# Optimization experiments

Measured on AMD Instinct MI355X. Metric: run time of the kernel, lower is better.

The kernel has to match this reference:

```python
import jax, jax.numpy as jnp
import numpy as np

CUTOFF = 4.0
D_RBF = 20


def _rbf_consts():
    # e3nn soft_one_hot_linspace, basis='gaussian', cutoff=False
    values = np.linspace(0.0, CUTOFF, D_RBF)
    step = values[1] - values[0]
    # RadialBasis normalization buffers: 4000 uniform samples, unbiased std
    rs = np.linspace(0.0, CUTOFF, 4001)[1:]
    bs = np.exp(-(((rs[:, None] - values[None, :]) / step) ** 2)) / 1.12
    mean = bs.mean(0)
    inv_std = 1.0 / bs.std(0, ddof=1)
    return (jnp.asarray(values, jnp.float32), jnp.float32(step),
            jnp.asarray(mean, jnp.float32), jnp.asarray(inv_std, jnp.float32))


def setup_inputs() -> dict:
    N, P, E = 2000, 50000, 300000
    Ds, Dv, H, HO = 256, 128, 256, 128
    din = Ds + Dv + D_RBF + Dv  # 532
    key = jax.random.key(0)
    ks = jax.random.split(key, 12)
    atom_xyz = jax.random.uniform(ks[0], (N, 3), jnp.float32, 0.0, 8.0)
    probe_xyz = jax.random.uniform(ks[1], (P, 3), jnp.float32, 0.0, 8.0)
    cell = jnp.eye(3, dtype=jnp.float32)[None] * 8.0  # [1,3,3]
    src = jax.random.randint(ks[2], (E,), 0, N)
    dst = jax.random.randint(ks[3], (E,), 0, P)
    edges = jnp.stack([src, dst], axis=-1).astype(jnp.int32)  # [E,2]
    edges_displacement = jax.random.randint(ks[4], (E, 3), -1, 2).astype(jnp.float32)
    S_final = jax.random.normal(ks[5], (N, Ds), jnp.float32)
    V_final = jax.random.normal(ks[6], (N, Dv, 3), jnp.float32)
    s = 0.02
    return {
        'atom_xyz': atom_xyz, 'probe_xyz': probe_xyz, 'cell': cell,
        'edges': edges, 'edges_displacement': edges_displacement,
        'S_final': S_final, 'V_final': V_final,
        'ln_gamma': jnp.ones((din,), jnp.float32),
        'ln_beta': jnp.zeros((din,), jnp.float32),
        'W1': jax.random.normal(ks[7], (din, H), jnp.float32) * s,
        'b1': jnp.zeros((H,), jnp.float32),
        'W2': jax.random.normal(ks[8], (H, H), jnp.float32) * s,
        'b2': jnp.zeros((H,), jnp.float32),
        'Wo1': jax.random.normal(ks[9], (H, HO), jnp.float32) * s,
        'bo1': jnp.zeros((HO,), jnp.float32),
        'Wo2': jax.random.normal(ks[10], (HO, 1), jnp.float32) * s,
        'bo2': jnp.full((1,), -10.0, jnp.float32),
    }


def reference(atom_xyz, probe_xyz, cell, edges, edges_displacement,
              S_final, V_final, ln_gamma, ln_beta,
              W1, b1, W2, b2, Wo1, bo1, Wo2, bo2):
    values, step, rbf_mean, rbf_inv_std = _rbf_consts()
    src, dst = edges[:, 0], edges[:, 1]
    # PBC displacement: edges_displacement @ cell (single graph -> cell[0])
    disp = edges_displacement @ cell[0]                     # [E,3]
    vec = probe_xyz[dst] - (atom_xyz[src] + disp)           # [E,3]
    d = jnp.maximum(jnp.linalg.norm(vec, axis=-1, keepdims=True), 1e-8)
    r_hat = vec / d                                         # [E,3]
    ds = d[:, 0]                                            # [E]
    # RBF (gaussian soft one-hot) + normalization
    diff = (ds[:, None] - values) / step
    e = (jnp.exp(-diff * diff) / 1.12 - rbf_mean) * rbf_inv_std  # [E,20]
    x = ds / CUTOFF
    x5 = x ** 5
    env = (1.0 - 21.0 * x5 + 35.0 * x5 * x - 15.0 * x5 * x * x)
    env = env * (ds < CUTOFF).astype(jnp.float32)           # [E]
    # geometric invariants
    q = jnp.einsum('ek,eck->ec', r_hat, V_final[src])       # [E,Dv]
    n_atom = jnp.linalg.norm(V_final, axis=-1)              # [N,Dv]
    feat = jnp.concatenate([S_final[src], n_atom[src], e, q], axis=-1)  # [E,532]
    # LayerNorm
    mu = feat.mean(-1, keepdims=True)
    var = feat.var(-1, keepdims=True)
    feat = (feat - mu) * jax.lax.rsqrt(var + 1e-5) * ln_gamma + ln_beta
    # message MLP
    h = jax.nn.silu(feat @ W1 + b1)
    h = jax.nn.silu(h @ W2 + b2)                            # [E,256]
    # envelope-weighted scatter-add to probes
    m_p = jax.ops.segment_sum(h * env[:, None], dst,
                              num_segments=probe_xyz.shape[0])  # [P,256]
    # output MLP
    o = jax.nn.silu(m_p @ Wo1 + bo1)
    rho = o @ Wo2 + bo2                                     # [P,1]
    return rho[:, 0]
```

## Files before the change

### kernel.cpp

```cpp
#include <hip/hip_runtime.h>
#include <hip/hip_bf16.h>
#include <hip/hip_fp16.h>

#define DIN 532
#define DRBF 20
#define EB 32

typedef __attribute__((ext_vector_type(8))) short s8v;
typedef __attribute__((ext_vector_type(4))) float f4v;

static __device__ __forceinline__ float silu_f(float x){
    return x * __builtin_amdgcn_rcpf(1.0f + __expf(-x));
}
static __device__ __forceinline__ short f2bf(float x){
    __hip_bfloat16 b = __float2bfloat16(x);
    return *(short*)&b;
}
static __device__ __forceinline__ s8v pack8(float4 f0, float4 f1){
    s8v r;
    r[0]=f2bf(f0.x); r[1]=f2bf(f0.y); r[2]=f2bf(f0.z); r[3]=f2bf(f0.w);
    r[4]=f2bf(f1.x); r[5]=f2bf(f1.y); r[6]=f2bf(f1.z); r[7]=f2bf(f1.w);
    return r;
}
static __device__ __forceinline__ s8v pack8p(const float* p){
    float4 f0 = *(const float4*)p, f1 = *(const float4*)(p + 4);
    return pack8(f0, f1);
}
static __device__ __forceinline__ bool detect_bf16(const void* cellraw){
    float c0 = ((const float*)cellraw)[0];
    return !(c0 > 7.5f && c0 < 8.5f);
}
static __device__ __forceinline__ float loadr(const void* p, bool isbf, long idx){
    if (isbf) return __bfloat162float(((const __hip_bfloat16*)p)[idx]);
    return ((const float*)p)[idx];
}

struct ConvArgs {
    const void* src[10];
    float*      dst[10];
    int         sz[10];
    int         total;
};

__global__ __launch_bounds__(256) void k_pre(ConvArgs ca,
    const void* W1r, const void* gammar, const void* betar, const void* b1r,
    const void* W2r, const void* Wo1r, const void* cellraw,
    float* Gpart, float* Bpart, float* rbfc,
    short* w1ef, short* w2f, short* w1f, short* wo1f)
{
    int b = blockIdx.x, t = threadIdx.x;
    bool isbf = detect_bf16(cellraw);
    if (b < 256){
        int stride = 256 * 256;
        for (int i = b*256 + t; i < ca.total; i += stride){
            int idx = i, k = 0;
            while (idx >= ca.sz[k]) { idx -= ca.sz[k]; k++; }
            float v = 0.0f;
            if (ca.src[k]) v = loadr(ca.src[k], isbf, idx);
            ca.dst[k][idx] = v;
        }
        return;
    }
    int pb = b - 256;
    if (pb < 17){
        int i0 = pb * 32, i1 = min(i0 + 32, DIN);
        float g = 0.0f, bb = 0.0f;
        for (int i = i0; i < i1; i++){
            float w  = loadr(W1r, isbf, (long)i*256 + t);
            g  += loadr(gammar, isbf, i) * w;
            bb += loadr(betar,  isbf, i) * w;
        }
        if (pb == 0) bb += loadr(b1r, isbf, t);
        Gpart[pb*256 + t] = g;
        Bpart[pb*256 + t] = bb;
        return;
    }
    if (pb == 17){
        __shared__ float ssum[DRBF][8], ssq[DRBF][8];
        if (t < 160){
            int m = t >> 3, c = t & 7;
            const float step = 4.0f/19.0f;
            float vm = step * m;
            float s = 0.0f, ss = 0.0f;
            for (int i = c*500 + 1; i <= c*500 + 500; i++){
                float r = 0.001f * (float)i;
                float u = (r - vm) / step;
                float bv = __expf(-u*u) * (1.0f/1.12f);
                s += bv; ss += bv*bv;
            }
            ssum[m][c] = s; ssq[m][c] = ss;
        }
        __syncthreads();
        if (t < DRBF){
            float s = 0.0f, ss = 0.0f;
            for (int c = 0; c < 8; c++){ s += ssum[t][c]; ss += ssq[t][c]; }
            float mean = s / 4000.0f;
            float var  = (ss - s*s/4000.0f) / 3999.0f;
            rbfc[t]        = mean;
            rbfc[DRBF + t] = rsqrtf(var);
        }
        return;
    }
    int wid = t >> 6, lane = t & 63;
    int q8 = (lane >> 4) * 8, nl = lane & 15;
    if (pb <= 21){
        int f = (pb - 18)*4 + wid;
        for (int j = 0; j < 8; j++){
            int kk = q8 + j;
            int n  = f*16 + nl;
            float v = (kk < DRBF)
                ? loadr(gammar, isbf, 384 + kk) * loadr(W1r, isbf, (long)(384 + kk)*256 + n)
                : 0.0f;
            w1ef[((f << 6) | lane)*8 + j] = f2bf(v);
        }
    } else if (pb <= 53){
        int f = (pb - 22)*4 + wid;
        int ks = f & 7;
        for (int j = 0; j < 8; j++){
            int kk = ks*32 + q8 + j;
            int n  = (f >> 3)*16 + nl;
            w2f[((f << 6) | lane)*8 + j] = f2bf(loadr(W2r, isbf, (long)kk*256 + n));
        }
    } else if (pb <= 117){
        int f = (pb - 54)*4 + wid;
        int ksg = f >> 4, ntg = f & 15;
        int base;
        if (ksg < 8)       base = ksg * 32;
        else if (ksg < 12) base = 256 + (ksg - 8) * 32;
        else               base = 404 + (ksg - 12) * 32;
        for (int j = 0; j < 8; j++){
            int kk = base + q8 + j;
            int n  = ntg*16 + nl;
            w1f[((f << 6) | lane)*8 + j] =
                f2bf(loadr(gammar, isbf, kk) * loadr(W1r, isbf, (long)kk*256 + n));
        }
    } else {
        int f = (pb - 118)*4 + wid;
        int ks = f & 7;
        for (int j = 0; j < 8; j++){
            int kk = ks*32 + q8 + j;
            int n  = (f >> 3)*16 + nl;
            wo1f[((f << 6) | lane)*8 + j] = f2bf(loadr(Wo1r, isbf, (long)kk*128 + n));
        }
    }
}

__global__ __launch_bounds__(256) void k_mid(
    const float* S, const float* V, const short* w1f, float4* AM,
    float* scal, int N,
    const int* edges, const void* edraw, const float* cell,
    const float* axyz, const float* pxyz,
    int* etot, int* flag, int2* esd, float4* geo, float* m_p,
    const void* cellraw, int E,
    const float* Gpart, const float* Bpart, float* Gv, float* Bb,
    int GA, int GG)
{
    int b = blockIdx.x, t = threadIdx.x;
    int wid = t >> 6, lane = t & 63;

    if (b < GA){
        __shared__ float Vxl[16][132], Vyl[16][132], Vzl[16][132], nll[16][132];
        int q = lane >> 4, ml = lane & 15;
        int a0 = b * 16;

        for (int a = 0; a < 16; a++){
            int atom = min(a0 + a, N - 1);
            if (t < 128){
                float x = V[(size_t)atom*384 + 3*t];
                float y = V[(size_t)atom*384 + 3*t + 1];
                float z = V[(size_t)atom*384 + 3*t + 2];
                Vxl[a][t] = x; Vyl[a][t] = y; Vzl[a][t] = z;
                nll[a][t] = sqrtf(x*x + y*y + z*z);
            }
        }
        __syncthreads();

        for (int a2 = 0; a2 < 4; a2++){
            int a = (wid << 2) + a2;
            int row = min(a0 + a, N - 1);
            float v[11];
            #pragma unroll
            for (int k = 0; k < 11; k++) v[k] = 0.0f;
            for (int e = lane; e < 256; e += 64){
                float s = S[(size_t)row*256 + e];
                v[0] += s; v[1] += s*s;
            }
            for (int e = lane; e < 128; e += 64){
                float n = nll[a][e], x = Vxl[a][e], y = Vyl[a][e], z = Vzl[a][e];
                v[0] += n;   v[1] += n*n;
                v[2] += x;   v[3] += y;   v[4] += z;
                v[5] += x*x; v[6] += x*y; v[7] += x*z;
                v[8] += y*y; v[9] += y*z; v[10] += z*z;
            }
            #pragma unroll
            for (int k = 0; k < 11; k++)
                for (int off2 = 32; off2 > 0; off2 >>= 1)
                    v[k] += __shfl_xor(v[k], off2, 64);
            if (lane == 0 && a0 + a < N)
                for (int k = 0; k < 11; k++) scal[(a0 + a)*12 + k] = v[k];
        }

        f4v zz = {0.0f, 0.0f, 0.0f, 0.0f};
        f4v aA1[4], aM0[4], aM1[4], aM2[4];
        #pragma unroll
        for (int nt = 0; nt < 4; nt++){ aA1[nt]=zz; aM0[nt]=zz; aM1[nt]=zz; aM2[nt]=zz; }

        int srow = min(a0 + ml, N - 1);
        #pragma unroll
        for (int ks = 0; ks < 8; ks++){
            s8v av = pack8p(&S[(size_t)srow*256 + ks*32 + q*8]);
            #pragma unroll
            for (int nt = 0; nt < 4; nt++){
                s8v bf = ((const s8v*)w1f)[(((ks << 4) | ((wid << 2) | nt)) << 6) | lane];
                aA1[nt] = __builtin_amdgcn_mfma_f32_16x16x32_bf16(av, bf, aA1[nt], 0, 0, 0);
            }
        }
        #pragma unroll
        for (int ks = 0; ks < 4; ks++){
            s8v av = pack8p(&nll[ml][ks*32 + q*8]);
            #pragma unroll
            for (int nt = 0; nt < 4; nt++){
                s8v bf = ((const s8v*)w1f)[((((8 + ks) << 4) | ((wid << 2) | nt)) << 6) | lane];
                aA1[nt] = __builtin_amdgcn_mfma_f32_16x16x32_bf16(av, bf, aA1[nt], 0, 0, 0);
            }
        }
        #pragma unroll
        for (int ks = 0; ks < 4; ks++){
            s8v ax = pack8p(&Vxl[ml][ks*32 + q*8]);
            s8v ay = pack8p(&Vyl[ml][ks*32 + q*8]);
            s8v az = pack8p(&Vzl[ml][ks*32 + q*8]);
            #pragma unroll
            for (int nt = 0; nt < 4; nt++){
                s8v bf = ((const s8v*)w1f)[((((12 + ks) << 4) | ((wid << 2) | nt)) << 6) | lane];
                aM0[nt] = __builtin_amdgcn_mfma_f32_16x16x32_bf16(ax, bf, aM0[nt], 0, 0, 0);
                aM1[nt] = __builtin_amdgcn_mfma_f32_16x16x32_bf16(ay, bf, aM1[nt], 0, 0, 0);
                aM2[nt] = __builtin_amdgcn_mfma_f32_16x16x32_bf16(az, bf, aM2[nt], 0, 0, 0);
            }
        }

        #pragma unroll
        for (int nt = 0; nt < 4; nt++){
            #pragma unroll
            for (int reg = 0; reg < 4; reg++){
                int atom = a0 + (q << 2) + reg;
                if (atom < N)
                    AM[(size_t)atom*256 + ((wid << 6) | (nt << 4) | ml)] =
                        make_float4(aA1[nt][reg], aM0[nt][reg], aM1[nt][reg], aM2[nt][reg]);
            }
        }
        return;
    }

    if (b < GA + GG){
        __shared__ int wcnt[4], wbase[4];
        bool isbf = detect_bf16(cellraw);
        float c0=cell[0],c1=cell[1],c2=cell[2],c3=cell[3],c4=cell[4];
        float c5=cell[5],c6=cell[6],c7=cell[7],c8=cell[8];
        int i = (b - GA)*256 + t;

        bool act = false;
        int s = 0, dd = 0;
        float r0 = 0.f, r1 = 0.f, r2 = 0.f, dn = 0.f;
        if (i < E){
            s = edges[2*i]; dd = edges[2*i + 1];
            float d0 = loadr(edraw, isbf, 3L*i);
            float d1 = loadr(edraw, isbf, 3L*i + 1);
            float d2 = loadr(edraw, isbf, 3L*i + 2);
            float dx = d0*c0 + d1*c3 + d2*c6;
            float dy = d0*c1 + d1*c4 + d2*c7;
            float dz = d0*c2 + d1*c5 + d2*c8;
            float vx = pxyz[3*dd]   - (axyz[3*s]   + dx);
            float vy = pxyz[3*dd+1] - (axyz[3*s+1] + dy);
            float vz = pxyz[3*dd+2] - (axyz[3*s+2] + dz);
            dn = fmaxf(sqrtf(vx*vx + vy*vy + vz*vz), 1e-8f);
            act = dn < 4.0f;
            float inv = __builtin_amdgcn_rcpf(dn);
            r0 = vx*inv; r1 = vy*inv; r2 = vz*inv;
        }
        unsigned long long mask = __ballot(act);
        if (lane == 0) wcnt[wid] = __popcll(mask);
        __syncthreads();
        if (t == 0){
            int tot = wcnt[0] + wcnt[1] + wcnt[2] + wcnt[3];
            int base = tot ? atomicAdd(etot, tot) : 0;
            int run = base;
            #pragma unroll
            for (int w2 = 0; w2 < 4; w2++){ wbase[w2] = run; run += wcnt[w2]; }
        }
        __syncthreads();
        if (act){
            int pos = wbase[wid] + __popcll(mask & ((1ULL << lane) - 1ULL));
            esd[pos] = make_int2(s, dd);
            geo[pos] = make_float4(r0, r1, r2, dn);
            if (atomicExch(&flag[dd], 1) == 0){
                float4 z = make_float4(0.f, 0.f, 0.f, 0.f);
                float4* p = (float4*)&m_p[(size_t)dd*256];
                #pragma unroll 4
                for (int k = 0; k < 64; k++) p[k] = z;
            }
        }
        return;
    }

    float g = 0.0f, bb = 0.0f;
    #pragma unroll
    for (int i = 0; i < 17; i++){
        g  += Gpart[i*256 + t];
        bb += Bpart[i*256 + t];
    }
    Gv[t] = g;
    Bb[t] = bb;
}

__global__ __launch_bounds__(256, 2) void k_edge(
    const int2* esd, const float4* geo, const int* etot, const float* scal,
    const float4* AM, const float* Gv, const float* Bb, const float* b2,
    const short* w1ef, const short* w2f, const float* rbfc, float* m_p)
{
    __shared__ float Gl[256], Bbl[256], b2l[256];
    __shared__ float rmean[DRBF], rinv[DRBF];
    __shared__ int   esrc[EB], edst[EB];
    __shared__ float rh0[EB], rh1[EB], rh2[EB], envv[EB], muv[EB], av[EB];
    __shared__ __align__(16) short ebfl[EB][32];
    __shared__ __align__(16) short afrag[2][8][64][8];

    int t = threadIdx.x, wid = t >> 6, lane = t & 63;
    int q = lane >> 4, ml_ = lane & 15;
    Gl[t] = Gv[t]; Bbl[t] = Bb[t]; b2l[t] = b2[t];
    if (t < DRBF){ rmean[t] = rbfc[t]; rinv[t] = rbfc[DRBF + t]; }
    __syncthreads();

    int Ea = etot[0];
    int ntiles = (Ea + EB - 1) / EB;

    for (int tile = blockIdx.x; tile < ntiles; tile += gridDim.x){
        if (t < EB){
            int epos = tile*EB + t;
            if (epos < Ea){
                int2 sd = esd[epos];
                float4 g = geo[epos];
                float r0 = g.x, r1 = g.y, r2 = g.z, dn = g.w;
                float x = dn * 0.25f;
                float x2 = x*x, x4 = x2*x2, x5 = x4*x;
                float env = 1.0f - 21.0f*x5 + 35.0f*x5*x - 15.0f*x5*x2;
                const float step = 4.0f/19.0f;
                float se = 0.0f, sse = 0.0f;
                for (int m = 0; m < DRBF; m++){
                    float u  = (dn - step*m) / step;
                    float bv = __expf(-u*u) * (1.0f/1.12f);
                    float em = (bv - rmean[m]) * rinv[m];
                    ebfl[t][m] = f2bf(em);
                    se += em; sse += em*em;
                }
                for (int m = DRBF; m < 32; m++) ebfl[t][m] = 0;
                const float* sc = &scal[sd.x*12];
                float sumq = r0*sc[2] + r1*sc[3] + r2*sc[4];
                float ssqq = r0*r0*sc[5] + r1*r1*sc[8] + r2*r2*sc[10]
                           + 2.0f*(r0*r1*sc[6] + r0*r2*sc[7] + r1*r2*sc[9]);
                float mu  = (sc[0] + se + sumq) * (1.0f/(float)DIN);
                float msq = (sc[1] + sse + ssqq) * (1.0f/(float)DIN);
                float a   = rsqrtf(fmaxf(msq - mu*mu, 0.0f) + 1e-5f);
                esrc[t] = sd.x; edst[t] = sd.y;
                rh0[t] = r0; rh1[t] = r1; rh2[t] = r2;
                envv[t] = env; muv[t] = mu; av[t] = a;
            } else {
                esrc[t] = 0; edst[t] = 0;
                rh0[t] = rh1[t] = rh2[t] = 0.0f;
                envv[t] = 0.0f; muv[t] = 0.0f; av[t] = 0.0f;
                for (int m = 0; m < 32; m++) ebfl[t][m] = 0;
            }
        }
        __syncthreads();

        f4v zz = {0.0f, 0.0f, 0.0f, 0.0f};
        f4v az[2][4];
        s8v ea0 = *(const s8v*)&ebfl[ml_][q*8];
        s8v ea1 = *(const s8v*)&ebfl[16 + ml_][q*8];
        #pragma unroll
        for (int nt = 0; nt < 4; nt++){
            s8v bw = ((const s8v*)w1ef)[(((wid << 2) | nt) << 6) | lane];
            az[0][nt] = __builtin_amdgcn_mfma_f32_16x16x32_bf16(ea0, bw, zz, 0, 0, 0);
            az[1][nt] = __builtin_amdgcn_mfma_f32_16x16x32_bf16(ea1, bw, zz, 0, 0, 0);
        }

        float gk[4], bbk[4];
        #pragma unroll
        for (int nt = 0; nt < 4; nt++){
            int k = (wid << 6) | (nt << 4) | ml_;
            gk[nt] = Gl[k]; bbk[nt] = Bbl[k];
        }
        #pragma unroll
        for (int mt = 0; mt < 2; mt++){
            #pragma unroll
            for (int reg = 0; reg < 4; reg++){
                int e_ = (mt << 4) | (q << 2) | reg;
                int s_ = esrc[e_];
                float r0 = rh0[e_], r1 = rh1[e_], r2 = rh2[e_];
                float mu = muv[e_], a_ = av[e_];
                const float4* AMr = &AM[(size_t)s_*256 + ((wid << 6) | ml_)];
                #pragma unroll
                for (int nt = 0; nt < 4; nt++){
                    float4 am = AMr[nt << 4];
                    float z = az[mt][nt][reg] + am.x + r0*am.y + r1*am.z + r2*am.w;
                    float y = a_*(z - mu*gk[nt]) + bbk[nt];
                    float h1 = silu_f(y);
                    int ks = (wid << 1) | (nt >> 1);
                    int col = ((nt & 1) << 4) | ml_;
                    int lanep = ((col >> 3) << 4) | (q << 2) | reg;
                    afrag[mt][ks][lanep][col & 7] = f2bf(h1);
                }
            }
        }
        __syncthreads();

        f4v acc[2][4];
        #pragma unroll
        for (int mt = 0; mt < 2; mt++)
            #pragma unroll
            for (int nt = 0; nt < 4; nt++) acc[mt][nt] = zz;
        #pragma unroll
        for (int ks = 0; ks < 8; ks++){
            s8v a0 = *(const s8v*)&afrag[0][ks][lane][0];
            s8v a1 = *(const s8v*)&afrag[1][ks][lane][0];
            #pragma unroll
            for (int nt = 0; nt < 4; nt++){
                s8v bf = ((const s8v*)w2f)[(((((wid << 2) | nt) << 3) | ks) << 6) | lane];
                acc[0][nt] = __builtin_amdgcn_mfma_f32_16x16x32_bf16(a0, bf, acc[0][nt], 0, 0, 0);
                acc[1][nt] = __builtin_amdgcn_mfma_f32_16x16x32_bf16(a1, bf, acc[1][nt], 0, 0, 0);
            }
        }

        float b2k[4];
        #pragma unroll
        for (int nt = 0; nt < 4; nt++) b2k[nt] = b2l[(wid << 6) | (nt << 4) | ml_];
        #pragma unroll
        for (int mt = 0; mt < 2; mt++){
            #pragma unroll
            for (int reg = 0; reg < 4; reg++){
                int e_ = (mt << 4) | (q << 2) | reg;
                float env = envv[e_];
                if (env != 0.0f){
                    int dd = edst[e_];
                    float* mrow = &m_p[(size_t)dd*256 + (wid << 6) + ml_];
                    #pragma unroll
                    for (int nt = 0; nt < 4; nt++){
                        float z2 = acc[mt][nt][reg] + b2k[nt];
                        atomicAdd(&mrow[nt << 4], silu_f(z2) * env);
                    }
                }
            }
        }
        __syncthreads();
    }
}

__global__ __launch_bounds__(256) void k_probe(
    const float* m_p, const int* flag, const short* wo1f, const float* bo1,
    const float* Wo2, const float* bo2, void* out, const void* cellraw, int P)
{
    int t = threadIdx.x, wid = t >> 6, lane = t & 63;
    int q = lane >> 4, ml = lane & 15;
    int p0 = blockIdx.x * 128 + wid * 32;
    const float4* mp4 = (const float4*)m_p;

    f4v zz = {0.0f, 0.0f, 0.0f, 0.0f};
    f4v acc[2][8];
    #pragma unroll
    for (int mt = 0; mt < 2; mt++)
        #pragma unroll
        for (int nt = 0; nt < 8; nt++) acc[mt][nt] = zz;

    int row0 = min(p0 + ml, P - 1);
    int row1 = min(p0 + 16 + ml, P - 1);
    bool f0 = flag[row0] != 0;
    bool f1 = flag[row1] != 0;
    s8v zero8 = {0,0,0,0,0,0,0,0};

    #pragma unroll
    for (int ks = 0; ks < 8; ks++){
        int c = ks*8 + q*2;
        s8v a0 = zero8, a1 = zero8;
        if (f0){
            float4 f00 = mp4[(size_t)row0*64 + c], f01 = mp4[(size_t)row0*64 + c + 1];
            a0 = pack8(f00, f01);
        }
        if (f1){
            float4 f10 = mp4[(size_t)row1*64 + c], f11 = mp4[(size_t)row1*64 + c + 1];
            a1 = pack8(f10, f11);
        }
        #pragma unroll
        for (int nt = 0; nt < 8; nt++){
            s8v bf = ((const s8v*)wo1f)[(((nt << 3) | ks) << 6) | lane];
            acc[0][nt] = __builtin_amdgcn_mfma_f32_16x16x32_bf16(a0, bf, acc[0][nt], 0, 0, 0);
            acc[1][nt] = __builtin_amdgcn_mfma_f32_16x16x32_bf16(a1, bf, acc[1][nt], 0, 0, 0);
        }
    }

    float bo1v[8], wo2v[8];
    #pragma unroll
    for (int nt = 0; nt < 8; nt++){
        int n = (nt << 4) | ml;
        bo1v[nt] = bo1[n];
        wo2v[nt] = Wo2[n];
    }
    bool isbf = detect_bf16(cellraw);
    float bo2v = bo2[0];

    #pragma unroll
    for (int mt = 0; mt < 2; mt++){
        #pragma unroll
        for (int reg = 0; reg < 4; reg++){
            float s = 0.0f;
            #pragma unroll
            for (int nt = 0; nt < 8; nt++)
                s += silu_f(acc[mt][nt][reg] + bo1v[nt]) * wo2v[nt];
            s += __shfl_xor(s, 1, 64);
            s += __shfl_xor(s, 2, 64);
            s += __shfl_xor(s, 4, 64);
            s += __shfl_xor(s, 8, 64);
            if (ml == 0){
                int p = p0 + (mt << 4) + (q << 2) + reg;
                if (p < P){
                    float rho = s + bo2v;
                    if (isbf) ((__hip_bfloat16*)out)[p] = __float2bfloat16(rho);
                    else      ((float*)out)[p] = rho;
                }
            }
        }
    }
}

extern "C" void kernel_launch(void* const* d_in, const int* in_sizes, int n_in,
                              void* d_out, int out_size, void* d_ws, size_t ws_size,
                              hipStream_t stream)
{
    const int N = in_sizes[0] / 3;
    const int P = in_sizes[1] / 3;
    const int E = in_sizes[3] / 2;

    float* w = (float*)d_ws;
    size_t off = 0;
    auto carve = [&](size_t n) -> float* {
        float* p = w + off;
        off += (n + 63) & ~(size_t)63;
        return p;
    };

    const int conv_din[9] = {6, 5, 1, 0, 12, 14, 15, 2, 16};
    float* cdst[9];
    int    csz[9];
    int total = 0;
    for (int k = 0; k < 9; k++){
        csz[k]  = in_sizes[conv_din[k]];
        cdst[k] = carve(csz[k]);
        total  += csz[k];
    }
    float* c_V     = cdst[0];
    float* c_S     = cdst[1];
    float* c_probe = cdst[2];
    float* c_atom  = cdst[3];
    float* c_b2    = cdst[4];
    float* c_bo1   = cdst[5];
    float* c_Wo2   = cdst[6];
    float* c_cell  = cdst[7];
    float* c_bo2   = cdst[8];

    float* rbfc  = carve(2 * DRBF);
    float* AMf   = carve((size_t)N * 256 * 4);
    float* scal  = carve((size_t)N * 12);
    float* w1ef  = carve(16 * 64 * 8 / 2);
    float* w2f   = carve(128 * 64 * 8 / 2);
    float* w1f   = carve(256 * 64 * 8 / 2);
    float* wo1f  = carve(64 * 64 * 8 / 2);
    float* m_p   = carve((size_t)P * 256);
    int*   etot  = (int*)carve(64);
    int*   flag  = (int*)carve(P);
    float* Gv    = carve(256);
    float* Bb    = carve(256);
    float* Gpart = carve(17 * 256);
    float* Bpart = carve(17 * 256);
    int*   esd   = (int*)carve((size_t)E * 2);
    float* geo   = carve((size_t)E * 4);

    ConvArgs ca;
    for (int k = 0; k < 9; k++){
        ca.src[k] = d_in[conv_din[k]];
        ca.dst[k] = cdst[k];
        ca.sz[k]  = csz[k];
    }
    ca.src[9] = nullptr;
    ca.dst[9] = (float*)etot;
    ca.sz[9]  = 64 + P;
    ca.total  = total + 64 + P;

    const int* d_edges = (const int*)d_in[3];
    const int GA = (N + 15) / 16;
    const int GG = (E + 255) / 256;

    k_pre<<<390, 256, 0, stream>>>(ca,
        d_in[9], d_in[7], d_in[8], d_in[10], d_in[11], d_in[13], d_in[2],
        Gpart, Bpart, rbfc,
        (short*)w1ef, (short*)w2f, (short*)w1f, (short*)wo1f);
    k_mid<<<GA + GG + 1, 256, 0, stream>>>(
        c_S, c_V, (const short*)w1f, (float4*)AMf, scal, N,
        d_edges, d_in[4], c_cell, c_atom, c_probe,
        etot, flag, (int2*)esd, (float4*)geo, m_p, d_in[2], E,
        Gpart, Bpart, Gv, Bb, GA, GG);
    k_edge<<<512, 256, 0, stream>>>(
        (const int2*)esd, (const float4*)geo, etot, scal,
        (const float4*)AMf, Gv, Bb, c_b2,
        (const short*)w1ef, (const short*)w2f, rbfc, m_p);
    k_probe<<<(P + 127) / 128, 256, 0, stream>>>(
        m_p, flag, (const short*)wo1f, c_bo1, c_Wo2, c_bo2, d_out, d_in[2], P);
}
```

Before: 196.0 us.

## Run k_mid with 1024-thread blocks and stage S rows in shared memory

Raises the k_mid block size from 256 to 1024 threads. The atom branch now uses 16 waves, each computing one 16-column MFMA tile and the row statistics for one atom. S rows are staged in shared memory so the statistics pass and the MFMA pass no longer both read S from global memory. The edge-compaction branch now handles 1024 edges per block, which cuts the number of blocks and global atomics. In exchange, per-block shared memory grows and barriers span more waves, which may lower occupancy.

```diff
diff --git a/kernel.cpp b/kernel.cpp
--- a/kernel.cpp
+++ b/kernel.cpp
@@ -145,7 +145,7 @@
     }
 }
 
-__global__ __launch_bounds__(256) void k_mid(
+__global__ __launch_bounds__(1024) void k_mid(
     const float* S, const float* V, const short* w1f, float4* AM,
     float* scal, int N,
     const int* edges, const void* edraw, const float* cell,
@@ -159,34 +159,41 @@
     int wid = t >> 6, lane = t & 63;
 
     if (b < GA){
+        __shared__ float Sl[16][260];
         __shared__ float Vxl[16][132], Vyl[16][132], Vzl[16][132], nll[16][132];
         int q = lane >> 4, ml = lane & 15;
         int a0 = b * 16;
 
-        for (int a = 0; a < 16; a++){
-            int atom = min(a0 + a, N - 1);
-            if (t < 128){
-                float x = V[(size_t)atom*384 + 3*t];
-                float y = V[(size_t)atom*384 + 3*t + 1];
-                float z = V[(size_t)atom*384 + 3*t + 2];
-                Vxl[a][t] = x; Vyl[a][t] = y; Vzl[a][t] = z;
-                nll[a][t] = sqrtf(x*x + y*y + z*z);
-            }
+        #pragma unroll
+        for (int rep = 0; rep < 4; rep++){
+            int i = rep*1024 + t;
+            int a = i >> 8, c = i & 255;
+            Sl[a][c] = S[(size_t)min(a0 + a, N - 1)*256 + c];
+        }
+        #pragma unroll
+        for (int rep = 0; rep < 2; rep++){
+            int i = rep*1024 + t;
+            int a = i >> 7, c = i & 127;
+            const float* vp = &V[(size_t)min(a0 + a, N - 1)*384 + 3*c];
+            float x = vp[0], y = vp[1], z = vp[2];
+            Vxl[a][c] = x; Vyl[a][c] = y; Vzl[a][c] = z;
+            nll[a][c] = sqrtf(x*x + y*y + z*z);
         }
         __syncthreads();
 
-        for (int a2 = 0; a2 < 4; a2++){
-            int a = (wid << 2) + a2;
-            int row = min(a0 + a, N - 1);
+        {
             float v[11];
             #pragma unroll
             for (int k = 0; k < 11; k++) v[k] = 0.0f;
-            for (int e = lane; e < 256; e += 64){
-                float s = S[(size_t)row*256 + e];
+            #pragma unroll
+            for (int e0 = 0; e0 < 256; e0 += 64){
+                float s = Sl[wid][e0 + lane];
                 v[0] += s; v[1] += s*s;
             }
-            for (int e = lane; e < 128; e += 64){
-                float n = nll[a][e], x = Vxl[a][e], y = Vyl[a][e], z = Vzl[a][e];
+            #pragma unroll
+            for (int e0 = 0; e0 < 128; e0 += 64){
+                int e = e0 + lane;
+                float n = nll[wid][e], x = Vxl[wid][e], y = Vyl[wid][e], z = Vzl[wid][e];
                 v[0] += n;   v[1] += n*n;
                 v[2] += x;   v[3] += y;   v[4] += z;
                 v[5] += x*x; v[6] += x*y; v[7] += x*z;
@@ -196,67 +203,52 @@
             for (int k = 0; k < 11; k++)
                 for (int off2 = 32; off2 > 0; off2 >>= 1)
                     v[k] += __shfl_xor(v[k], off2, 64);
-            if (lane == 0 && a0 + a < N)
-                for (int k = 0; k < 11; k++) scal[(a0 + a)*12 + k] = v[k];
+            if (lane == 0 && a0 + wid < N)
+                for (int k = 0; k < 11; k++) scal[(a0 + wid)*12 + k] = v[k];
         }
 
         f4v zz = {0.0f, 0.0f, 0.0f, 0.0f};
-        f4v aA1[4], aM0[4], aM1[4], aM2[4];
-        #pragma unroll
-        for (int nt = 0; nt < 4; nt++){ aA1[nt]=zz; aM0[nt]=zz; aM1[nt]=zz; aM2[nt]=zz; }
-
-        int srow = min(a0 + ml, N - 1);
+        f4v aA1 = zz, aM0 = zz, aM1 = zz, aM2 = zz;
+
         #pragma unroll
         for (int ks = 0; ks < 8; ks++){
-            s8v av = pack8p(&S[(size_t)srow*256 + ks*32 + q*8]);
-            #pragma unroll
-            for (int nt = 0; nt < 4; nt++){
-                s8v bf = ((const s8v*)w1f)[(((ks << 4) | ((wid << 2) | nt)) << 6) | lane];
-                aA1[nt] = __builtin_amdgcn_mfma_f32_16x16x32_bf16(av, bf, aA1[nt], 0, 0, 0);
-            }
+            s8v av = pack8p(&Sl[ml][ks*32 + q*8]);
+            s8v bf = ((const s8v*)w1f)[(((ks << 4) | wid) << 6) | lane];
+            aA1 = __builtin_amdgcn_mfma_f32_16x16x32_bf16(av, bf, aA1, 0, 0, 0);
         }
         #pragma unroll
         for (int ks = 0; ks < 4; ks++){
             s8v av = pack8p(&nll[ml][ks*32 + q*8]);
-            #pragma unroll
-            for (int nt = 0; nt < 4; nt++){
-                s8v bf = ((const s8v*)w1f)[((((8 + ks) << 4) | ((wid << 2) | nt)) << 6) | lane];
-                aA1[nt] = __builtin_amdgcn_mfma_f32_16x16x32_bf16(av, bf, aA1[nt], 0, 0, 0);
-            }
+            s8v bf = ((const s8v*)w1f)[((((8 + ks) << 4) | wid) << 6) | lane];
+            aA1 = __builtin_amdgcn_mfma_f32_16x16x32_bf16(av, bf, aA1, 0, 0, 0);
         }
         #pragma unroll
         for (int ks = 0; ks < 4; ks++){
             s8v ax = pack8p(&Vxl[ml][ks*32 + q*8]);
             s8v ay = pack8p(&Vyl[ml][ks*32 + q*8]);
             s8v az = pack8p(&Vzl[ml][ks*32 + q*8]);
-            #pragma unroll
-            for (int nt = 0; nt < 4; nt++){
-                s8v bf = ((const s8v*)w1f)[((((12 + ks) << 4) | ((wid << 2) | nt)) << 6) | lane];
-                aM0[nt] = __builtin_amdgcn_mfma_f32_16x16x32_bf16(ax, bf, aM0[nt], 0, 0, 0);
-                aM1[nt] = __builtin_amdgcn_mfma_f32_16x16x32_bf16(ay, bf, aM1[nt], 0, 0, 0);
-                aM2[nt] = __builtin_amdgcn_mfma_f32_16x16x32_bf16(az, bf, aM2[nt], 0, 0, 0);
-            }
-        }
-
-        #pragma unroll
-        for (int nt = 0; nt < 4; nt++){
-            #pragma unroll
-            for (int reg = 0; reg < 4; reg++){
-                int atom = a0 + (q << 2) + reg;
-                if (atom < N)
-                    AM[(size_t)atom*256 + ((wid << 6) | (nt << 4) | ml)] =
-                        make_float4(aA1[nt][reg], aM0[nt][reg], aM1[nt][reg], aM2[nt][reg]);
-            }
+            s8v bf = ((const s8v*)w1f)[((((12 + ks) << 4) | wid) << 6) | lane];
+            aM0 = __builtin_amdgcn_mfma_f32_16x16x32_bf16(ax, bf, aM0, 0, 0, 0);
+            aM1 = __builtin_amdgcn_mfma_f32_16x16x32_bf16(ay, bf, aM1, 0, 0, 0);
+            aM2 = __builtin_amdgcn_mfma_f32_16x16x32_bf16(az, bf, aM2, 0, 0, 0);
+        }
+
+        #pragma unroll
+        for (int reg = 0; reg < 4; reg++){
+            int atom = a0 + (q << 2) + reg;
+            if (atom < N)
+                AM[(size_t)atom*256 + ((wid << 4) | ml)] =
+                    make_float4(aA1[reg], aM0[reg], aM1[reg], aM2[reg]);
         }
         return;
     }
 
     if (b < GA + GG){
-        __shared__ int wcnt[4], wbase[4];
+        __shared__ int wcnt[16], wbase[16];
         bool isbf = detect_bf16(cellraw);
         float c0=cell[0],c1=cell[1],c2=cell[2],c3=cell[3],c4=cell[4];
         float c5=cell[5],c6=cell[6],c7=cell[7],c8=cell[8];
-        int i = (b - GA)*256 + t;
+        int i = (b - GA)*1024 + t;
 
         bool act = false;
         int s = 0, dd = 0;
@@ -281,11 +273,13 @@
         if (lane == 0) wcnt[wid] = __popcll(mask);
         __syncthreads();
         if (t == 0){
-            int tot = wcnt[0] + wcnt[1] + wcnt[2] + wcnt[3];
+            int tot = 0;
+            #pragma unroll
+            for (int w2 = 0; w2 < 16; w2++) tot += wcnt[w2];
             int base = tot ? atomicAdd(etot, tot) : 0;
             int run = base;
             #pragma unroll
-            for (int w2 = 0; w2 < 4; w2++){ wbase[w2] = run; run += wcnt[w2]; }
+            for (int w2 = 0; w2 < 16; w2++){ wbase[w2] = run; run += wcnt[w2]; }
         }
         __syncthreads();
         if (act){
@@ -302,14 +296,16 @@
         return;
     }
 
-    float g = 0.0f, bb = 0.0f;
-    #pragma unroll
-    for (int i = 0; i < 17; i++){
-        g  += Gpart[i*256 + t];
-        bb += Bpart[i*256 + t];
-    }
-    Gv[t] = g;
-    Bb[t] = bb;
+    if (t < 256){
+        float g = 0.0f, bb = 0.0f;
+        #pragma unroll
+        for (int i = 0; i < 17; i++){
+            g  += Gpart[i*256 + t];
+            bb += Bpart[i*256 + t];
+        }
+        Gv[t] = g;
+        Bb[t] = bb;
+    }
 }
 
 __global__ __launch_bounds__(256, 2) void k_edge(
@@ -595,13 +591,13 @@
 
     const int* d_edges = (const int*)d_in[3];
     const int GA = (N + 15) / 16;
-    const int GG = (E + 255) / 256;
+    const int GG = (E + 1023) / 1024;
 
     k_pre<<<390, 256, 0, stream>>>(ca,
         d_in[9], d_in[7], d_in[8], d_in[10], d_in[11], d_in[13], d_in[2],
         Gpart, Bpart, rbfc,
         (short*)w1ef, (short*)w2f, (short*)w1f, (short*)wo1f);
-    k_mid<<<GA + GG + 1, 256, 0, stream>>>(
+    k_mid<<<GA + GG + 1, 1024, 0, stream>>>(
         c_S, c_V, (const short*)w1f, (float4*)AMf, scal, N,
         d_edges, d_in[4], c_cell, c_atom, c_probe,
         etot, flag, (int2*)esd, (float4*)geo, m_p, d_in[2], E,
```

After: 177.6 us, median of 2. 1.1x faster.
